# Performance work log

Hardware: AMD Instinct MI355X
Metric: run time of the kernel (lower is better)

## Reference

```python
import jax, jax.numpy as jnp
import numpy as np
import math

# Dims: d_model=192, expand=2 -> d_inner=d_ssm=384, headdim=64 -> nheads=6,
# d_state=128, K=4 scan directions, ngroups=1 (directions fused into state dim).
D_MODEL = 192
D_STATE = 128
D_CONV = 3
EXPAND = 2
HEADDIM = 64
CHUNK = 256
D_INNER = EXPAND * D_MODEL          # 384
D_SSM = D_INNER                     # default d_ssm (d_mlp == 0)
NHEADS = D_SSM // HEADDIM           # 6
K = 4                               # scan directions
HTOT = K * NHEADS                   # 24 heads in the fused scan
NSTATE = K * D_STATE                # 512 fused state dim (ngroups=1)
CONV_BC = 2 * D_STATE + NHEADS      # 262
B, H, W = 2, 64, 64


def _dwconv(x, w, b):
    # x: (B,C,H,W), w: (C,1,k,k) depthwise, SAME padding ((k-1)//2)
    y = jax.lax.conv_general_dilated(
        x, w, (1, 1), [(1, 1), (1, 1)],
        feature_group_count=x.shape[1],
        dimension_numbers=('NCHW', 'OIHW', 'NCHW'))
    return y + b[None, :, None, None]


def _ssd(x, dt_raw, A_logs, Bm, Cm, Ds, dt_bias):
    # Mamba2 chunked selective scan (dt_softplus=True, default dt_limit).
    # x: (b,l,h,p)  dt_raw: (b,l,h)  Bm,Cm: (b,l,n) with ngroups=1
    A = -jnp.exp(A_logs)                              # (h,)
    dt = jax.nn.softplus(dt_raw + dt_bias)            # (b,l,h)
    b, l, h, p = x.shape
    n = Bm.shape[-1]
    nc = l // CHUNK
    xc = x.reshape(b, nc, CHUNK, h, p)
    dtc = dt.reshape(b, nc, CHUNK, h)
    Bc = Bm.reshape(b, nc, CHUNK, n)
    Cc = Cm.reshape(b, nc, CHUNK, n)
    dA = dtc * A                                      # (b,nc,cs,h)
    acum = jnp.cumsum(dA, axis=2)
    # intra-chunk (causal, attention-like)
    a_t = jnp.transpose(acum, (0, 1, 3, 2))           # (b,nc,h,cs)
    diff = a_t[..., :, None] - a_t[..., None, :]      # (b,nc,h,i,j)
    causal = jnp.tril(jnp.ones((CHUNK, CHUNK), bool))
    Lmat = jnp.where(causal, jnp.exp(diff), 0.0)
    CB = jnp.einsum('bcin,bcjn->bcij', Cc, Bc)        # (b,nc,i,j)
    M = CB[:, :, None] * Lmat * jnp.transpose(dtc, (0, 1, 3, 2))[:, :, :, None, :]
    y = jnp.einsum('bchij,bcjhp->bcihp', M, xc)
    # chunk-final states
    decay_end = jnp.exp(acum[:, :, -1:, :] - acum)    # (b,nc,cs,h)
    states = jnp.einsum('bcjh,bcjn,bcjhp->bchpn', decay_end * dtc, Bc, xc)
    chunk_decay = jnp.exp(acum[:, :, -1, :])          # (b,nc,h)

    def step(S, inp):
        st, dec = inp
        return S * dec[:, :, None, None] + st, S

    S0 = jnp.zeros((b, h, p, n), x.dtype)
    _, prev = jax.lax.scan(step, S0, (jnp.moveaxis(states, 1, 0),
                                      jnp.moveaxis(chunk_decay, 1, 0)))
    prev = jnp.moveaxis(prev, 0, 1)                   # (b,nc,h,p,n)
    y = y + jnp.einsum('bcih,bcin,bchpn->bcihp', jnp.exp(acum), Cc, prev)
    y = y + xc * Ds[:, None]                          # D skip connection
    return y.reshape(b, l, h, p)


def _branch(u, u_cross, W_skip, W_xs, W_bcdt, conv_xs_w, conv_xs_b,
            conv_bc_w, conv_bc_b, dt_bias, A_logs, Ds, norm_w, W_out):
    Bb, Hh, Ww, _ = u.shape
    L = Hh * Ww
    z = (u @ W_skip).reshape(Bb, L, D_SSM)            # gate (d_mlp == 0)
    xs = jnp.transpose(u @ W_xs, (0, 3, 1, 2))        # (B,d_ssm,H,W)
    xs = jax.nn.silu(_dwconv(xs, conv_xs_w, conv_xs_b))
    bc = jnp.transpose(u_cross @ W_bcdt, (0, 3, 1, 2))
    bc = jax.nn.silu(_dwconv(bc, conv_bc_w, conv_bc_b))
    xbc = jnp.concatenate([xs, bc], axis=1)           # (B,646,H,W)
    C = xbc.shape[1]
    v = xbc.reshape(Bb, C, L)                         # HW raster
    vt = jnp.transpose(xbc, (0, 1, 3, 2)).reshape(Bb, C, L)  # WH raster
    hw = jnp.stack([v, vt], axis=1)                   # (B,2,C,L)
    xbcdt = jnp.concatenate([hw, jnp.flip(hw, axis=-1)], axis=1)  # (B,4,C,L)
    xp = xbcdt[:, :, :D_SSM]
    Bp = xbcdt[:, :, D_SSM:D_SSM + D_STATE]
    Cp = xbcdt[:, :, D_SSM + D_STATE:D_SSM + 2 * D_STATE]
    dtp = xbcdt[:, :, D_SSM + 2 * D_STATE:]
    x = xp.reshape(Bb, K * D_SSM, L).transpose(0, 2, 1).reshape(Bb, L, HTOT, HEADDIM)
    Bm = Bp.reshape(Bb, NSTATE, L).transpose(0, 2, 1)
    Cm = Cp.reshape(Bb, NSTATE, L).transpose(0, 2, 1)
    dt = dtp.reshape(Bb, HTOT, L).transpose(0, 2, 1)
    y = _ssd(x, dt, A_logs, Bm, Cm, Ds, dt_bias)      # (B,L,24,64)
    y = y.reshape(Bb, L, K, D_SSM)
    out_y = y[:, :, 0]
    inv_y = jnp.flip(y[:, :, 2:4], axis=1)            # (B,L,2,d_ssm)
    wh_y = y[:, :, 1].reshape(Bb, Ww, Hh, D_SSM).transpose(0, 2, 1, 3).reshape(Bb, L, D_SSM)
    invwh_y = inv_y[:, :, 1].reshape(Bb, Ww, Hh, D_SSM).transpose(0, 2, 1, 3).reshape(Bb, L, D_SSM)
    yf = out_y + inv_y[:, :, 0] + wh_y + invwh_y
    # gated RMSNorm (norm_before_gate=False, group_size == d_ssm)
    g = yf * jax.nn.silu(z)
    g = g * jax.lax.rsqrt(jnp.mean(g * g, axis=-1, keepdims=True) + 1e-5) * norm_w
    return (g @ W_out).reshape(Bb, Hh, Ww, D_MODEL)


def setup_inputs():
    key = jax.random.key(0)
    ks = jax.random.split(key, 16)
    f = lambda i, s: jax.random.normal(ks[i], s, jnp.float32)
    sc = 0.02
    dt = jnp.exp(jax.random.uniform(ks[10], (NHEADS,)) *
                 (math.log(0.1) - math.log(0.001)) + math.log(0.001))
    dt = jnp.maximum(dt, 1e-4)
    inv_dt = dt + jnp.log(-jnp.expm1(-dt))
    A = jax.random.uniform(ks[11], (NHEADS,), minval=1.0, maxval=16.0)
    return {
        'u1': f(0, (B, H, W, D_MODEL)),
        'u2': f(1, (B, H, W, D_MODEL)),
        'u2_cat_u1': f(2, (B, H, W, D_MODEL)),
        'u1_cat_u2': f(3, (B, H, W, D_MODEL)),
        'W_skip': f(4, (D_MODEL, D_SSM)) * sc,
        'W_xs': f(5, (D_MODEL, D_SSM)) * sc,
        'W_bcdt': f(6, (D_MODEL, CONV_BC)) * sc,
        'conv_xs_w': f(7, (D_SSM, 1, D_CONV, D_CONV)) * sc,
        'conv_xs_b': jnp.zeros((D_SSM,), jnp.float32),
        'conv_bc_w': f(8, (CONV_BC, 1, D_CONV, D_CONV)) * sc,
        'conv_bc_b': jnp.zeros((CONV_BC,), jnp.float32),
        'dt_bias': jnp.tile(inv_dt, K),
        'A_logs': jnp.tile(jnp.log(A), K),
        'Ds': jnp.ones((HTOT,), jnp.float32),
        'norm_w': jnp.ones((D_SSM,), jnp.float32),
        'W_out': f(9, (D_SSM, D_MODEL)) * sc,
    }


def reference(u1, u2, u2_cat_u1, u1_cat_u2, W_skip, W_xs, W_bcdt,
              conv_xs_w, conv_xs_b, conv_bc_w, conv_bc_b,
              dt_bias, A_logs, Ds, norm_w, W_out):
    args = (W_skip, W_xs, W_bcdt, conv_xs_w, conv_xs_b, conv_bc_w,
            conv_bc_b, dt_bias, A_logs, Ds, norm_w, W_out)
    out1 = _branch(u1, u2_cat_u1, *args)
    out2 = _branch(u2, u1_cat_u2, *args)
    return out1, out2
```

## Files before the change

kernel.cpp:

```cpp
#include <hip/hip_runtime.h>
#include <hip/hip_bf16.h>

#define DEV __device__ __forceinline__

static constexpr int LL   = 4096;
static constexpr int GG   = 4;
static constexpr int CBC  = 262;
static constexpr int BSTR = 264;

typedef float f32x4  __attribute__((ext_vector_type(4)));
typedef short bf16x8 __attribute__((ext_vector_type(8)));
typedef short bf16x4v __attribute__((ext_vector_type(4)));

DEV int map_l(int s, int k) {
    int m = (k & 2) ? (4095 - s) : s;
    if (k & 1) m = ((m & 63) << 6) | (m >> 6);
    return m;
}
DEV float silu_f(float x) { return x / (1.f + __expf(-x)); }
DEV short f2bf(float f) {
    union { __hip_bfloat16 h; short s; } u;
    u.h = __float2bfloat16(f);
    return u.s;
}
DEV float bf2f(short s) {
    return __uint_as_float(((unsigned)(unsigned short)s) << 16);
}
DEV bf16x8 pack8(float4 a, float4 b) {
    bf16x8 r;
    r[0]=f2bf(a.x); r[1]=f2bf(a.y); r[2]=f2bf(a.z); r[3]=f2bf(a.w);
    r[4]=f2bf(b.x); r[5]=f2bf(b.y); r[6]=f2bf(b.z); r[7]=f2bf(b.w);
    return r;
}
DEV bf16x8 load8u(const __hip_bfloat16* p) {
    bf16x4v lo = *(const bf16x4v*)p;
    bf16x4v hi = *(const bf16x4v*)(p + 4);
    bf16x8 r;
    r[0]=lo[0]; r[1]=lo[1]; r[2]=lo[2]; r[3]=lo[3];
    r[4]=hi[0]; r[5]=hi[1]; r[6]=hi[2]; r[7]=hi[3];
    return r;
}
DEV void store16(__hip_bfloat16* p, const float* v) {
    bf16x8 a, b;
    #pragma unroll
    for (int e = 0; e < 8; ++e) { a[e] = f2bf(v[e]); b[e] = f2bf(v[8+e]); }
    *(bf16x8*)p = a;
    *((bf16x8*)p + 1) = b;
}
DEV void storeT(float v, float* p) { *p = v; }
DEV void storeT(float v, __hip_bfloat16* p) { *p = __float2bfloat16(v); }

__global__ void sentinel_k(float* out) { out[0] = 1e30f; }

__global__ void wt_all_k(const float* __restrict__ W_skip, const float* __restrict__ W_xs,
                         const float* __restrict__ W_bcdt, const float* __restrict__ W_out,
                         __hip_bfloat16* __restrict__ Wt)
{
    int idx = blockIdx.x * 256 + threadIdx.x;
    if (idx < 73728) {
        int n = idx / 192, k = idx - n * 192;
        Wt[idx] = __float2bfloat16(W_skip[(size_t)k * 384 + n]);
    } else if (idx < 147456) {
        int r = idx - 73728;
        int n = r / 192, k = r - n * 192;
        Wt[idx] = __float2bfloat16(W_xs[(size_t)k * 384 + n]);
    } else if (idx < 208896) {
        int r = idx - 147456;
        int n = r / 192, k = r - n * 192;
        Wt[idx] = __float2bfloat16(n < 262 ? W_bcdt[(size_t)k * 262 + n] : 0.f);
    } else if (idx < 282624) {
        int r = idx - 208896;
        int n = r / 384, k = r - n * 384;
        Wt[idx] = __float2bfloat16(W_out[(size_t)k * 192 + n]);
    }
}

template<int MODE, typename AT, typename OutT>
__global__ __launch_bounds__(256) void mgemm_k(
    const AT* __restrict__ A0, const AT* __restrict__ A1,
    const __hip_bfloat16* __restrict__ Wt, OutT* __restrict__ C,
    OutT* __restrict__ C2, int N, int Kd)
{
    int i0 = blockIdx.y * 128;
    int j0 = blockIdx.x * 64;
    int t = threadIdx.x;
    int w = t >> 6, lane = t & 63;
    int lr = lane & 15, kq = lane >> 4;
    const AT* arow[2];
    #pragma unroll
    for (int a = 0; a < 2; ++a) {
        int grow = i0 + w * 32 + a * 16 + lr;
        const AT* Ap = (grow < 8192) ? A0 : A1;
        arow[a] = Ap + (size_t)(grow & 8191) * Kd;
    }
    f32x4 acc[2][4] = {};
    for (int k0 = 0; k0 < Kd; k0 += 32) {
        int kb = k0 + kq * 8;
        bf16x8 af[2];
        #pragma unroll
        for (int a = 0; a < 2; ++a) {
            if constexpr (sizeof(AT) == 4)
                af[a] = pack8(*(const float4*)(arow[a] + kb), *(const float4*)(arow[a] + kb + 4));
            else
                af[a] = *(const bf16x8*)(arow[a] + kb);
        }
        #pragma unroll
        for (int b = 0; b < 4; ++b) {
            int n = j0 + b * 16 + lr;
            bf16x8 bfr = *(const bf16x8*)(Wt + (size_t)n * Kd + kb);
            #pragma unroll
            for (int a = 0; a < 2; ++a)
                acc[a][b] = __builtin_amdgcn_mfma_f32_16x16x32_bf16(af[a], bfr, acc[a][b], 0, 0, 0);
        }
    }
    #pragma unroll
    for (int a = 0; a < 2; ++a)
        #pragma unroll
        for (int b = 0; b < 4; ++b)
            #pragma unroll
            for (int r = 0; r < 4; ++r) {
                int row = i0 + w * 32 + a * 16 + kq * 4 + r;
                int col = j0 + b * 16 + lr;
                float v = acc[a][b][r];
                if constexpr (MODE == 0) {
                    if (col < N) storeT(v, &C[(size_t)row * N + col]);
                } else if constexpr (MODE == 1) {
                    if (col < N) storeT(silu_f(v), &C[(size_t)row * N + col]);
                } else {
                    if (col < 384) storeT(silu_f(v), &C[(size_t)row * 384 + col]);
                    else           storeT(v, &C2[(size_t)row * 384 + col - 384]);
                }
            }
}

template<typename InT, typename OutT>
__global__ void dwconv_k(const InT* __restrict__ in, const float* __restrict__ w,
                         const float* __restrict__ bias, OutT* __restrict__ out,
                         int Cin, int Cout)
{
    int idx = blockIdx.x * 256 + threadIdx.x;
    int total = GG * LL * Cin;
    if (idx >= total) return;
    int c = idx % Cin;
    int l = (idx / Cin) % LL;
    int g = idx / (Cin * LL);
    int h = l >> 6, ww = l & 63;
    float acc = bias[c];
    #pragma unroll
    for (int dy = 0; dy < 3; ++dy) {
        int hh = h + dy - 1;
        if ((unsigned)hh >= 64u) continue;
        #pragma unroll
        for (int dx = 0; dx < 3; ++dx) {
            int wx = ww + dx - 1;
            if ((unsigned)wx >= 64u) continue;
            float iv;
            if constexpr (sizeof(InT) == 4) iv = in[((size_t)g * LL + (hh << 6) + wx) * Cin + c];
            else iv = __bfloat162float(in[((size_t)g * LL + (hh << 6) + wx) * Cin + c]);
            acc += iv * w[c * 9 + dy * 3 + dx];
        }
    }
    storeT(silu_f(acc), &out[((size_t)g * LL + l) * Cout + c]);
}

__global__ __launch_bounds__(256) void xtc_k(const __hip_bfloat16* __restrict__ pre_xs,
                                             const float* __restrict__ cxw,
                                             const float* __restrict__ cxb,
                                             __hip_bfloat16* __restrict__ XtG)
{
    __shared__ float raw[18][18][17];
    __shared__ float ls[16][17][17];
    __shared__ float wsm[16][9];
    __shared__ float bsm[16];
    int bid = blockIdx.x;
    int pct = bid % 24;
    int rest = bid / 24;
    int wt = rest & 3, ht2 = (rest >> 2) & 3, g = rest >> 4;
    int h0 = ht2 * 16, w0 = wt * 16, pc0 = pct * 16;
    int t = threadIdx.x;
    if (t < 144) wsm[t / 9][t % 9] = cxw[(pc0 + t / 9) * 9 + t % 9];
    if (t < 16)  bsm[t] = cxb[pc0 + t];
    for (int i = t; i < 18 * 18 * 16; i += 256) {
        int ch = i & 15;
        int hw = i >> 4;
        int ww2 = hw % 18, hh = hw / 18;
        int gh = h0 - 1 + hh, gw = w0 - 1 + ww2;
        float v = 0.f;
        if ((unsigned)gh < 64u && (unsigned)gw < 64u)
            v = __bfloat162float(pre_xs[((size_t)g * LL + gh * 64 + gw) * 384 + pc0 + ch]);
        raw[hh][ww2][ch] = v;
    }
    __syncthreads();
    {
        int h = t >> 4, w2 = t & 15;
        #pragma unroll 4
        for (int ch = 0; ch < 16; ++ch) {
            float acc = bsm[ch];
            #pragma unroll
            for (int dy = 0; dy < 3; ++dy)
                #pragma unroll
                for (int dx = 0; dx < 3; ++dx)
                    acc += raw[h + dy][w2 + dx][ch] * wsm[ch][dy * 3 + dx];
            ls[h][w2][ch] = silu_f(acc);
        }
    }
    __syncthreads();
    int pc = t >> 4, q = t & 15;
    float v[16];
    size_t rowbase;
    #pragma unroll
    for (int e = 0; e < 16; ++e) v[e] = ls[q][e][pc];
    rowbase = ((size_t)(g * 2 + 0) * 384 + pc0 + pc) * 4096;
    store16(XtG + rowbase + (h0 + q) * 64 + w0, v);
    #pragma unroll
    for (int e = 0; e < 16; ++e) v[e] = ls[e][q][pc];
    rowbase = ((size_t)(g * 2 + 1) * 384 + pc0 + pc) * 4096;
    store16(XtG + rowbase + (w0 + q) * 64 + h0, v);
}

__global__ __launch_bounds__(256) void bt_k(const float* __restrict__ bct,
                                            __hip_bfloat16* __restrict__ Bt)
{
    __shared__ float ls[16][17][17];
    int bid = blockIdx.x;
    int nt = bid & 31;
    int rest = bid >> 5;
    int wt = rest & 3, ht2 = (rest >> 2) & 3, g = rest >> 4;
    int h0 = ht2 * 16, w0 = wt * 16;
    int kd = nt >> 3, ch0 = (nt & 7) * 16;
    int t = threadIdx.x;
    int cl = t & 15, hwb = t >> 4;
    #pragma unroll
    for (int r = 0; r < 16; ++r) {
        int hw = hwb + r * 16;
        int h = hw >> 4, w2 = hw & 15;
        ls[h][w2][cl] = bct[((size_t)g * LL + (h0 + h) * 64 + (w0 + w2)) * BSTR + ch0 + cl];
    }
    __syncthreads();
    int pc = t >> 4, q = t & 15;
    int n = nt * 16 + pc;
    __hip_bfloat16* rowp = Bt + ((size_t)g * 512 + n) * 4096;
    float v[16];
    if (kd == 0) {
        #pragma unroll
        for (int e = 0; e < 16; ++e) v[e] = ls[q][e][pc];
        store16(rowp + (h0 + q) * 64 + w0, v);
    } else if (kd == 1) {
        #pragma unroll
        for (int e = 0; e < 16; ++e) v[e] = ls[e][q][pc];
        store16(rowp + (w0 + q) * 64 + h0, v);
    } else if (kd == 2) {
        #pragma unroll
        for (int e = 0; e < 16; ++e) v[e] = ls[q][15 - e][pc];
        store16(rowp + 4095 - (h0 + q) * 64 - w0 - 15, v);
    } else {
        #pragma unroll
        for (int e = 0; e < 16; ++e) v[e] = ls[15 - e][q][pc];
        store16(rowp + 4095 - (w0 + q) * 64 - h0 - 15, v);
    }
}

__global__ __launch_bounds__(256) void cs_k(const float* __restrict__ bct,
                                            __hip_bfloat16* __restrict__ Cs)
{
    __shared__ float ls[16][16][17];
    int bid = blockIdx.x;
    int ct = bid & 15;
    int rest = bid >> 4;
    int wt = rest & 3, ht2 = (rest >> 2) & 3, g = rest >> 4;
    int h0 = ht2 * 16, w0 = wt * 16;
    int kd = ct >> 3, ch0 = (ct & 7) * 16;
    int t = threadIdx.x;
    int cl = t & 15, hwb = t >> 4;
    #pragma unroll
    for (int r = 0; r < 16; ++r) {
        int hw = hwb + r * 16;
        int h = hw >> 4, w2 = hw & 15;
        ls[h][w2][cl] = bct[((size_t)g * LL + (h0 + h) * 64 + (w0 + w2)) * BSTR + 128 + ch0 + cl];
    }
    __syncthreads();
    int h = t >> 4, w2 = t & 15;
    int s = (kd == 0) ? (h0 + h) * 64 + (w0 + w2) : (w0 + w2) * 64 + (h0 + h);
    float v[16];
    #pragma unroll
    for (int e = 0; e < 16; ++e) v[e] = ls[h][w2][e];
    store16(Cs + ((size_t)g * 4096 + s) * 256 + kd * 128 + ch0, v);
}

__global__ __launch_bounds__(256) void dtscan_k(
    const float* __restrict__ bct, const float* __restrict__ dt_bias,
    const float* __restrict__ A_logs, float* __restrict__ dt_arr,
    float* __restrict__ ac_arr, float* __restrict__ cdecay)
{
    int bid = blockIdx.x;
    int ht = bid % 24;
    int gc = bid / 24;
    int c = gc & 15, g = gc >> 4;
    int k = ht / 6, h = ht % 6;
    int t = threadIdx.x;
    int s = c * 256 + t;
    int l = map_l(s, k);
    float raw = bct[((size_t)g * LL + l) * BSTR + 256 + h] + dt_bias[ht];
    float dtv = raw > 20.f ? raw : log1pf(__expf(raw));
    float dA = dtv * (-__expf(A_logs[ht]));
    float v = dA;
    #pragma unroll
    for (int off = 1; off < 64; off <<= 1) {
        float u = __shfl_up(v, off);
        if ((t & 63) >= off) v += u;
    }
    __shared__ float wsum[4];
    if ((t & 63) == 63) wsum[t >> 6] = v;
    __syncthreads();
    float add = 0.f;
    #pragma unroll
    for (int w2 = 0; w2 < 3; ++w2)
        if (w2 < (t >> 6)) add += wsum[w2];
    float cum = v + add;
    size_t base = ((size_t)g * 24 + ht) * LL + s;
    dt_arr[base] = dtv;
    ac_arr[base] = cum;
    if (t == 255) cdecay[(g * 24 + ht) * 16 + c] = __expf(cum);
}

__global__ __launch_bounds__(256) void cb_k(const float* __restrict__ bct,
                                            const __hip_bfloat16* __restrict__ Cs,
                                            __hip_bfloat16* __restrict__ CBm)
{
    int bid = blockIdx.x;
    int jq = bid & 3;
    int gc = bid >> 2;
    int c = gc & 15, g = gc >> 4;
    int t = threadIdx.x;
    int w = t >> 6, lane = t & 63;
    int lr = lane & 15, kq = lane >> 4;
    const float* bg = bct + (size_t)g * LL * BSTR;
    const __hip_bfloat16* cg = Cs + (size_t)g * 4096 * 256;
    f32x4 acc[4][4] = {};
    for (int ks = 0; ks < 16; ++ks) {
        int n0 = ks * 32 + kq * 8;
        int kd = n0 >> 7, nn = n0 & 127;
        bf16x8 bfr[4];
        #pragma unroll
        for (int jt = 0; jt < 4; ++jt) {
            int j = jq * 64 + jt * 16 + lr;
            int l = map_l(c * 256 + j, kd);
            const float* p = bg + (size_t)l * BSTR + nn;
            bfr[jt] = pack8(*(const float4*)p, *(const float4*)(p + 4));
        }
        #pragma unroll
        for (int iq = 0; iq < 4; ++iq) {
            int i = (w * 4 + iq) * 16 + lr;
            int s = c * 256 + i;
            int row = (kd < 2) ? s : 4095 - s;
            int col = ((kd & 1) << 7) + nn;
            bf16x8 af = *(const bf16x8*)(cg + (size_t)row * 256 + col);
            #pragma unroll
            for (int jt = 0; jt < 4; ++jt)
                acc[iq][jt] = __builtin_amdgcn_mfma_f32_16x16x32_bf16(af, bfr[jt], acc[iq][jt], 0, 0, 0);
        }
    }
    __hip_bfloat16* ob = CBm + (size_t)gc * 65536;
    #pragma unroll
    for (int iq = 0; iq < 4; ++iq)
        #pragma unroll
        for (int jt = 0; jt < 4; ++jt)
            #pragma unroll
            for (int r = 0; r < 4; ++r) {
                int i = (w * 4 + iq) * 16 + kq * 4 + r;
                int j = jq * 64 + jt * 16 + lr;
                ob[(size_t)i * 256 + j] = __float2bfloat16(acc[iq][jt][r]);
            }
}

__global__ __launch_bounds__(256) void states_k(
    const __hip_bfloat16* __restrict__ XtG, const __hip_bfloat16* __restrict__ Bt,
    const float* __restrict__ dt_arr, const float* __restrict__ ac_arr,
    __hip_bfloat16* __restrict__ states)
{
    __shared__ float wsh[256];
    __shared__ short xw[64][264];
    int task = (blockIdx.x & 7) * 192 + (blockIdx.x >> 3);
    int ht = task % 24;
    int gc = task / 24;
    int c = gc & 15, g = gc >> 4;
    int kd = ht / 6;
    bool rev = kd >= 2;
    int c0 = (ht % 6) * 64;
    int t = threadIdx.x;
    int w = t >> 6, lane = t & 63;
    int lr = lane & 15, kq = lane >> 4;
    const float* dtp = dt_arr + ((size_t)g * 24 + ht) * LL + c * 256;
    const float* acp = ac_arr + ((size_t)g * 24 + ht) * LL + c * 256;
    float ac_last = acp[255];
    wsh[t] = __expf(ac_last - acp[t]) * dtp[t];
    __syncthreads();
    const __hip_bfloat16* xg = XtG + ((size_t)(g * 2 + (kd & 1)) * 384 + c0) * 4096;
    #pragma unroll
    for (int r8 = 0; r8 < 8; ++r8) {
        int id = t + 256 * r8;
        int p = id >> 5;
        int jc = (id & 31) * 8;
        bf16x8 xv;
        if (!rev) {
            xv = *(const bf16x8*)(xg + (size_t)p * 4096 + c * 256 + jc);
        } else {
            bf16x8 tmp = load8u(xg + (size_t)p * 4096 + 4088 - c * 256 - jc);
            #pragma unroll
            for (int e = 0; e < 8; ++e) xv[e] = tmp[7 - e];
        }
        bf16x8 o;
        #pragma unroll
        for (int e = 0; e < 8; ++e) o[e] = f2bf(bf2f(xv[e]) * wsh[jc + e]);
        *(bf16x8*)&xw[p][jc] = o;
    }
    __syncthreads();
    const __hip_bfloat16* btg = Bt + (size_t)g * 512 * 4096;
    f32x4 acc[4][8] = {};
    for (int ks = 0; ks < 8; ++ks) {
        int j0 = ks * 32 + kq * 8;
        bf16x8 af[4];
        #pragma unroll
        for (int pt = 0; pt < 4; ++pt)
            af[pt] = *(const bf16x8*)&xw[pt * 16 + lr][j0];
        #pragma unroll
        for (int nt = 0; nt < 8; ++nt) {
            int n = (w * 8 + nt) * 16 + lr;
            bf16x8 bv = *(const bf16x8*)(btg + (size_t)n * 4096 + c * 256 + j0);
            #pragma unroll
            for (int pt = 0; pt < 4; ++pt)
                acc[pt][nt] = __builtin_amdgcn_mfma_f32_16x16x32_bf16(af[pt], bv, acc[pt][nt], 0, 0, 0);
        }
    }
    __hip_bfloat16* ob = states + ((size_t)gc * 24 + ht) * 32768;
    #pragma unroll
    for (int pt = 0; pt < 4; ++pt)
        #pragma unroll
        for (int nt = 0; nt < 8; ++nt)
            #pragma unroll
            for (int r = 0; r < 4; ++r) {
                int p = pt * 16 + kq * 4 + r;
                int n = (w * 8 + nt) * 16 + lr;
                ob[(size_t)p * 512 + n] = __float2bfloat16(acc[pt][nt][r]);
            }
}

__global__ void scan_k(__hip_bfloat16* __restrict__ states, const float* __restrict__ cdecay)
{
    int idx = blockIdx.x * 256 + threadIdx.x;
    int g = idx / 786432;
    int r = idx - g * 786432;
    int ht = r >> 15;
    int pn = r & 32767;
    const float* cd = cdecay + (g * 24 + ht) * 16;
    __hip_bfloat16* base = states + ((size_t)g * 384 + ht) * 32768 + pn;
    float S = 0.f;
    #pragma unroll
    for (int c2 = 0; c2 < 16; ++c2) {
        __hip_bfloat16* p = base + (size_t)c2 * 786432;
        float tmp = __bfloat162float(*p);
        *p = __float2bfloat16(S);
        S = S * cd[c2] + tmp;
    }
}

__global__ __launch_bounds__(256) void yk(
    const __hip_bfloat16* __restrict__ XtG, const __hip_bfloat16* __restrict__ Cs,
    const __hip_bfloat16* __restrict__ CBm, const __hip_bfloat16* __restrict__ prev,
    const float* __restrict__ dt_arr, const float* __restrict__ ac_arr,
    const float* __restrict__ Ds, __hip_bfloat16* __restrict__ y4)
{
    __shared__ float acs[256], dts[256], ejdt[256];
    __shared__ short xl[64][264];
    int task = (blockIdx.x & 7) * 192 + (blockIdx.x >> 3);
    int ht = task % 24;
    int gc = task / 24;
    int c = gc & 15, g = gc >> 4;
    int kd = ht / 6;
    bool rev = kd >= 2;
    int c0 = (ht % 6) * 64;
    int t = threadIdx.x;
    int w = t >> 6, lane = t & 63;
    int lr = lane & 15, kq = lane >> 4;
    acs[t] = ac_arr[((size_t)g * 24 + ht) * LL + c * 256 + t];
    dts[t] = dt_arr[((size_t)g * 24 + ht) * LL + c * 256 + t];
    const __hip_bfloat16* xg = XtG + ((size_t)(g * 2 + (kd & 1)) * 384 + c0) * 4096;
    #pragma unroll
    for (int r8 = 0; r8 < 8; ++r8) {
        int id = t + 256 * r8;
        int p = id >> 5;
        int jc = (id & 31) * 8;
        bf16x8 xv;
        if (!rev) {
            xv = *(const bf16x8*)(xg + (size_t)p * 4096 + c * 256 + jc);
        } else {
            bf16x8 tmp = load8u(xg + (size_t)p * 4096 + 4088 - c * 256 - jc);
            #pragma unroll
            for (int e = 0; e < 8; ++e) xv[e] = tmp[7 - e];
        }
        *(bf16x8*)&xl[p][jc] = xv;
    }
    __syncthreads();
    ejdt[t] = __expf(acs[t & ~31] - acs[t]) * dts[t];
    __syncthreads();
    const __hip_bfloat16* cbb = CBm + (size_t)gc * 65536;
    const __hip_bfloat16* cg = Cs + (size_t)g * 4096 * 256;
    f32x4 acc[4][4] = {};
    const __hip_bfloat16* pv = prev + ((size_t)gc * 24 + ht) * 32768;
    auto ld2 = [&](int ns, bf16x8* afq, bf16x8* pb) {
        int n0 = ns * 32 + kq * 8;
        int kd2 = n0 >> 7, nn = n0 & 127;
        int col = ((kd2 & 1) << 7) + nn;
        #pragma unroll
        for (int q = 0; q < 4; ++q) {
            int i = (w + 4 * q) * 16 + lr;
            int s = c * 256 + i;
            int row = (kd2 < 2) ? s : 4095 - s;
            afq[q] = *(const bf16x8*)(cg + (size_t)row * 256 + col);
        }
        #pragma unroll
        for (int pt = 0; pt < 4; ++pt)
            pb[pt] = *(const bf16x8*)(pv + (size_t)(pt * 16 + lr) * 512 + n0);
    };
    auto fma2 = [&](bf16x8* afq, bf16x8* pb) {
        #pragma unroll
        for (int q = 0; q < 4; ++q)
            #pragma unroll
            for (int pt = 0; pt < 4; ++pt)
                acc[q][pt] = __builtin_amdgcn_mfma_f32_16x16x32_bf16(afq[q], pb[pt], acc[q][pt], 0, 0, 0);
    };
    {
        bf16x8 afA[4], pbA[4], afB[4], pbB[4];
        ld2(0, afA, pbA);
        #pragma unroll
        for (int ns = 0; ns < 16; ns += 2) {
            if (ns + 1 < 16) ld2(ns + 1, afB, pbB);
            fma2(afA, pbA);
            if (ns + 2 < 16) ld2(ns + 2, afA, pbA);
            fma2(afB, pbB);
        }
    }
    #pragma unroll
    for (int q = 0; q < 4; ++q)
        #pragma unroll
        for (int r = 0; r < 4; ++r) {
            float er = __expf(acs[(w + 4 * q) * 16 + kq * 4 + r]);
            #pragma unroll
            for (int pt = 0; pt < 4; ++pt) acc[q][pt][r] *= er;
        }
    float aci_q[4];
    #pragma unroll
    for (int q = 0; q < 4; ++q) aci_q[q] = acs[(w + 4 * q) * 16 + lr];
    for (int ks = 0; ks < 8; ++ks) {
        int j0 = ks * 32 + kq * 8;
        bf16x8 xb[4];
        #pragma unroll
        for (int pt = 0; pt < 4; ++pt)
            xb[pt] = *(const bf16x8*)&xl[pt * 16 + lr][j0];
        float acb = acs[ks * 32];
        float ej[8];
        #pragma unroll
        for (int e = 0; e < 8; ++e) ej[e] = ejdt[j0 + e];
        #pragma unroll
        for (int q = 0; q < 4; ++q) {
            int rt = w + 4 * q;
            if (rt < 2 * ks) continue;
            int i = rt * 16 + lr;
            float r2 = __expf(aci_q[q] - acb);
            bf16x8 cb8 = *(const bf16x8*)(cbb + (size_t)i * 256 + j0);
            bf16x8 af;
            if (rt >= 2 * ks + 2) {
                #pragma unroll
                for (int e = 0; e < 8; ++e)
                    af[e] = f2bf(r2 * ej[e] * bf2f(cb8[e]));
            } else {
                #pragma unroll
                for (int e = 0; e < 8; ++e) {
                    float coef = r2 * ej[e] * bf2f(cb8[e]);
                    af[e] = (j0 + e <= i) ? f2bf(coef) : (short)0;
                }
            }
            #pragma unroll
            for (int pt = 0; pt < 4; ++pt)
                acc[q][pt] = __builtin_amdgcn_mfma_f32_16x16x32_bf16(af, xb[pt], acc[q][pt], 0, 0, 0);
        }
    }
    float Dsv = Ds[ht];
    __hip_bfloat16* yb = y4 + (((size_t)(g * 4 + kd) * 4096 + c * 256) * 384) + c0;
    #pragma unroll
    for (int q = 0; q < 4; ++q) {
        int rt = w + 4 * q;
        #pragma unroll
        for (int pt = 0; pt < 4; ++pt) {
            int p = pt * 16 + lr;
            int ibase = rt * 16 + kq * 4;
            bf16x4v x4 = *(const bf16x4v*)&xl[p][ibase];
            #pragma unroll
            for (int r = 0; r < 4; ++r) {
                int i = ibase + r;
                float xv = bf2f(x4[r]);
                yb[(size_t)i * 384 + p] = __float2bfloat16(acc[q][pt][r] + Dsv * xv);
            }
        }
    }
}

__global__ __launch_bounds__(128) void gate_k(
    const __hip_bfloat16* __restrict__ y4, const __hip_bfloat16* __restrict__ z_silu,
    const float* __restrict__ norm_w, __hip_bfloat16* __restrict__ gn)
{
    int g = blockIdx.x >> 12;
    int l = blockIdx.x & 4095;
    int t = threadIdx.x;
    int Tl = ((l & 63) << 6) | (l >> 6);
    const __hip_bfloat16* p0 = y4 + ((size_t)(g * 4 + 0) * 4096 + l) * 384;
    const __hip_bfloat16* p1 = y4 + ((size_t)(g * 4 + 1) * 4096 + Tl) * 384;
    const __hip_bfloat16* p2 = y4 + ((size_t)(g * 4 + 2) * 4096 + 4095 - l) * 384;
    const __hip_bfloat16* p3 = y4 + ((size_t)(g * 4 + 3) * 4096 + 4095 - Tl) * 384;
    const __hip_bfloat16* zp = z_silu + ((size_t)g * LL + l) * 384;
    float gc[3]; float ssq = 0.f;
    #pragma unroll
    for (int q = 0; q < 3; ++q) {
        int cdim = t + 128 * q;
        float yf = __bfloat162float(p0[cdim]) + __bfloat162float(p1[cdim]) +
                   __bfloat162float(p2[cdim]) + __bfloat162float(p3[cdim]);
        float v = yf * __bfloat162float(zp[cdim]);
        gc[q] = v;
        ssq += v * v;
    }
    float v = ssq;
    #pragma unroll
    for (int off = 32; off > 0; off >>= 1) v += __shfl_down(v, off);
    __shared__ float tot[2];
    if ((t & 63) == 0) tot[t >> 6] = v;
    __syncthreads();
    float rs = rsqrtf((tot[0] + tot[1]) * (1.f / 384.f) + 1e-5f);
    __hip_bfloat16* gp = gn + ((size_t)g * LL + l) * 384;
    #pragma unroll
    for (int q = 0; q < 3; ++q) {
        int cdim = t + 128 * q;
        gp[cdim] = __float2bfloat16(gc[q] * rs * norm_w[cdim]);
    }
}

extern "C" void kernel_launch(void* const* d_in, const int* in_sizes, int n_in,
                              void* d_out, int out_size, void* d_ws, size_t ws_size,
                              hipStream_t stream)
{
    const float* u1      = (const float*)d_in[0];
    const float* u2      = (const float*)d_in[1];
    const float* u21     = (const float*)d_in[2];
    const float* u12     = (const float*)d_in[3];
    const float* W_skip  = (const float*)d_in[4];
    const float* W_xs    = (const float*)d_in[5];
    const float* W_bcdt  = (const float*)d_in[6];
    const float* cxw     = (const float*)d_in[7];
    const float* cxb     = (const float*)d_in[8];
    const float* cbw     = (const float*)d_in[9];
    const float* cbb     = (const float*)d_in[10];
    const float* dt_bias = (const float*)d_in[11];
    const float* A_logs  = (const float*)d_in[12];
    const float* Ds      = (const float*)d_in[13];
    const float* norm_w  = (const float*)d_in[14];
    const float* W_out   = (const float*)d_in[15];
    float* out = (float*)d_out;

    char* w = (char*)d_ws;
    size_t o_y4  = 0;
    size_t o_st  = o_y4 + 50331648;
    size_t o_z   = o_st + 100663296;
    size_t o_xtg = o_z  + 12582912;
    size_t o_bt  = o_xtg + 25165824;
    size_t o_cs  = o_bt + 16777216;
    size_t o_cbm = o_cs + 8388608;
    size_t o_dt  = o_cbm + 8388608;
    size_t o_ac  = o_dt + 1572864;
    size_t o_cd  = o_ac + 1572864;
    size_t o_wt  = o_cd + 8192;
    size_t total = o_wt + 589824;
    if (total > ws_size) {
        sentinel_k<<<1, 1, 0, stream>>>(out);
        return;
    }
    __hip_bfloat16* y4     = (__hip_bfloat16*)(w + o_y4);
    __hip_bfloat16* states = (__hip_bfloat16*)(w + o_st);
    __hip_bfloat16* z_silu = (__hip_bfloat16*)(w + o_z);
    __hip_bfloat16* XtG    = (__hip_bfloat16*)(w + o_xtg);
    __hip_bfloat16* Bt     = (__hip_bfloat16*)(w + o_bt);
    __hip_bfloat16* Cs     = (__hip_bfloat16*)(w + o_cs);
    __hip_bfloat16* CBm    = (__hip_bfloat16*)(w + o_cbm);
    float*          dt_arr = (float*)(w + o_dt);
    float*          ac_arr = (float*)(w + o_ac);
    float*          cdecay = (float*)(w + o_cd);
    __hip_bfloat16* Wt     = (__hip_bfloat16*)(w + o_wt);
    __hip_bfloat16* Wt_skip = Wt;
    __hip_bfloat16* Wt_bcdt = Wt + 147456;
    __hip_bfloat16* Wt_out  = Wt + 208896;
    float*          bct    = (float*)(w + o_y4);
    __hip_bfloat16* pre_bc = (__hip_bfloat16*)(w + o_st);
    __hip_bfloat16* pre_xs = (__hip_bfloat16*)(w + o_st + 8650752);
    __hip_bfloat16* gn     = (__hip_bfloat16*)(w + o_st);

    dim3 blk(256);
    wt_all_k<<<dim3(1104), blk, 0, stream>>>(W_skip, W_xs, W_bcdt, W_out, Wt);
    mgemm_k<2, float, __hip_bfloat16><<<dim3(12, 128), blk, 0, stream>>>(
        u1, u2, Wt_skip, z_silu, pre_xs, 768, 192);
    mgemm_k<0, float, __hip_bfloat16><<<dim3(5, 128), blk, 0, stream>>>(
        u21, u12, Wt_bcdt, pre_bc, nullptr, CBC, 192);
    dwconv_k<__hip_bfloat16, float><<<dim3((GG * LL * CBC) / 256), blk, 0, stream>>>(
        pre_bc, cbw, cbb, bct, CBC, BSTR);
    xtc_k<<<dim3(1536), blk, 0, stream>>>(pre_xs, cxw, cxb, XtG);
    bt_k<<<dim3(2048), blk, 0, stream>>>(bct, Bt);
    cs_k<<<dim3(1024), blk, 0, stream>>>(bct, Cs);
    dtscan_k<<<dim3(1536), blk, 0, stream>>>(bct, dt_bias, A_logs, dt_arr, ac_arr, cdecay);
    cb_k<<<dim3(256), blk, 0, stream>>>(bct, Cs, CBm);
    states_k<<<dim3(1536), blk, 0, stream>>>(XtG, Bt, dt_arr, ac_arr, states);
    scan_k<<<dim3(12288), blk, 0, stream>>>(states, cdecay);
    yk<<<dim3(1536), blk, 0, stream>>>(XtG, Cs, CBm, states, dt_arr, ac_arr, Ds, y4);
    gate_k<<<dim3(16384), dim3(128), 0, stream>>>(y4, z_silu, norm_w, gn);
    mgemm_k<0, __hip_bfloat16, float><<<dim3(3, 128), blk, 0, stream>>>(
        gn, gn + (size_t)8192 * 384, Wt_out, out, nullptr, 192, 384);
}
```

Measured before the change: 459.5 us.

## Fuse B/C transpose and dt-scan prep kernels; add bf16 B layout for CB GEMM

Merges bt_k, cs_k and dtscan_k into a single prep_k launch selected by block index, and has it also write a bf16 copy of B in the same row layout as C. cb_k then reads contiguous bf16 vectors instead of gathering scattered fp32 rows through map_l. In states_k and yk the X loads are issued earlier into registers so they overlap with the dt/ac loads, and yk computes the chunk-base cumsum with a shuffle, dropping one barrier. In exchange it needs an extra 8 MB workspace buffer and more register pressure from holding X in registers.

```diff
diff --git a/kernel.cpp b/kernel.cpp
--- a/kernel.cpp
+++ b/kernel.cpp
@@ -218,113 +218,110 @@
     store16(XtG + rowbase + (w0 + q) * 64 + h0, v);
 }
 
-__global__ __launch_bounds__(256) void bt_k(const float* __restrict__ bct,
-                                            __hip_bfloat16* __restrict__ Bt)
+__global__ __launch_bounds__(256) void prep_k(
+    const float* __restrict__ bct, const float* __restrict__ dt_bias,
+    const float* __restrict__ A_logs, __hip_bfloat16* __restrict__ Bt,
+    __hip_bfloat16* __restrict__ Cs, __hip_bfloat16* __restrict__ Bs,
+    float* __restrict__ dt_arr, float* __restrict__ ac_arr,
+    float* __restrict__ cdecay)
 {
     __shared__ float ls[16][17][17];
+    __shared__ float wsum[4];
     int bid = blockIdx.x;
-    int nt = bid & 31;
-    int rest = bid >> 5;
-    int wt = rest & 3, ht2 = (rest >> 2) & 3, g = rest >> 4;
-    int h0 = ht2 * 16, w0 = wt * 16;
-    int kd = nt >> 3, ch0 = (nt & 7) * 16;
     int t = threadIdx.x;
-    int cl = t & 15, hwb = t >> 4;
-    #pragma unroll
-    for (int r = 0; r < 16; ++r) {
-        int hw = hwb + r * 16;
-        int h = hw >> 4, w2 = hw & 15;
-        ls[h][w2][cl] = bct[((size_t)g * LL + (h0 + h) * 64 + (w0 + w2)) * BSTR + ch0 + cl];
-    }
-    __syncthreads();
-    int pc = t >> 4, q = t & 15;
-    int n = nt * 16 + pc;
-    __hip_bfloat16* rowp = Bt + ((size_t)g * 512 + n) * 4096;
-    float v[16];
-    if (kd == 0) {
-        #pragma unroll
-        for (int e = 0; e < 16; ++e) v[e] = ls[q][e][pc];
-        store16(rowp + (h0 + q) * 64 + w0, v);
-    } else if (kd == 1) {
-        #pragma unroll
-        for (int e = 0; e < 16; ++e) v[e] = ls[e][q][pc];
-        store16(rowp + (w0 + q) * 64 + h0, v);
-    } else if (kd == 2) {
-        #pragma unroll
-        for (int e = 0; e < 16; ++e) v[e] = ls[q][15 - e][pc];
-        store16(rowp + 4095 - (h0 + q) * 64 - w0 - 15, v);
+    if (bid < 2048) {
+        int nt = bid & 31;
+        int rest = bid >> 5;
+        int wt = rest & 3, ht2 = (rest >> 2) & 3, g = rest >> 4;
+        int h0 = ht2 * 16, w0 = wt * 16;
+        int kd = nt >> 3, ch0 = (nt & 7) * 16;
+        int cl = t & 15, hwb = t >> 4;
+        #pragma unroll
+        for (int r = 0; r < 16; ++r) {
+            int hw = hwb + r * 16;
+            int h = hw >> 4, w2 = hw & 15;
+            ls[h][w2][cl] = bct[((size_t)g * LL + (h0 + h) * 64 + (w0 + w2)) * BSTR + ch0 + cl];
+        }
+        __syncthreads();
+        int pc = t >> 4, q = t & 15;
+        int n = nt * 16 + pc;
+        __hip_bfloat16* rowp = Bt + ((size_t)g * 512 + n) * 4096;
+        float v[16];
+        if (kd == 0) {
+            #pragma unroll
+            for (int e = 0; e < 16; ++e) v[e] = ls[q][e][pc];
+            store16(rowp + (h0 + q) * 64 + w0, v);
+        } else if (kd == 1) {
+            #pragma unroll
+            for (int e = 0; e < 16; ++e) v[e] = ls[e][q][pc];
+            store16(rowp + (w0 + q) * 64 + h0, v);
+        } else if (kd == 2) {
+            #pragma unroll
+            for (int e = 0; e < 16; ++e) v[e] = ls[q][15 - e][pc];
+            store16(rowp + 4095 - (h0 + q) * 64 - w0 - 15, v);
+        } else {
+            #pragma unroll
+            for (int e = 0; e < 16; ++e) v[e] = ls[15 - e][q][pc];
+            store16(rowp + 4095 - (w0 + q) * 64 - h0 - 15, v);
+        }
+    } else if (bid < 4096) {
+        int b2 = bid - 2048;
+        int ct = b2 & 31;
+        int rest = b2 >> 5;
+        int wt = rest & 3, ht2 = (rest >> 2) & 3, g = rest >> 4;
+        int h0 = ht2 * 16, w0 = wt * 16;
+        bool isB = ct >= 16;
+        int ctl = ct & 15;
+        int kd = ctl >> 3, ch0 = (ctl & 7) * 16;
+        int off = (isB ? 0 : 128) + ch0;
+        __hip_bfloat16* dst = isB ? Bs : Cs;
+        int cl = t & 15, hwb = t >> 4;
+        #pragma unroll
+        for (int r = 0; r < 16; ++r) {
+            int hw = hwb + r * 16;
+            int h = hw >> 4, w2 = hw & 15;
+            ls[h][w2][cl] = bct[((size_t)g * LL + (h0 + h) * 64 + (w0 + w2)) * BSTR + off + cl];
+        }
+        __syncthreads();
+        int h = t >> 4, w2 = t & 15;
+        int s = (kd == 0) ? (h0 + h) * 64 + (w0 + w2) : (w0 + w2) * 64 + (h0 + h);
+        float v[16];
+        #pragma unroll
+        for (int e = 0; e < 16; ++e) v[e] = ls[h][w2][e];
+        store16(dst + ((size_t)g * 4096 + s) * 256 + kd * 128 + ch0, v);
     } else {
-        #pragma unroll
-        for (int e = 0; e < 16; ++e) v[e] = ls[15 - e][q][pc];
-        store16(rowp + 4095 - (w0 + q) * 64 - h0 - 15, v);
-    }
-}
-
-__global__ __launch_bounds__(256) void cs_k(const float* __restrict__ bct,
-                                            __hip_bfloat16* __restrict__ Cs)
-{
-    __shared__ float ls[16][16][17];
-    int bid = blockIdx.x;
-    int ct = bid & 15;
-    int rest = bid >> 4;
-    int wt = rest & 3, ht2 = (rest >> 2) & 3, g = rest >> 4;
-    int h0 = ht2 * 16, w0 = wt * 16;
-    int kd = ct >> 3, ch0 = (ct & 7) * 16;
-    int t = threadIdx.x;
-    int cl = t & 15, hwb = t >> 4;
-    #pragma unroll
-    for (int r = 0; r < 16; ++r) {
-        int hw = hwb + r * 16;
-        int h = hw >> 4, w2 = hw & 15;
-        ls[h][w2][cl] = bct[((size_t)g * LL + (h0 + h) * 64 + (w0 + w2)) * BSTR + 128 + ch0 + cl];
-    }
-    __syncthreads();
-    int h = t >> 4, w2 = t & 15;
-    int s = (kd == 0) ? (h0 + h) * 64 + (w0 + w2) : (w0 + w2) * 64 + (h0 + h);
-    float v[16];
-    #pragma unroll
-    for (int e = 0; e < 16; ++e) v[e] = ls[h][w2][e];
-    store16(Cs + ((size_t)g * 4096 + s) * 256 + kd * 128 + ch0, v);
-}
-
-__global__ __launch_bounds__(256) void dtscan_k(
-    const float* __restrict__ bct, const float* __restrict__ dt_bias,
-    const float* __restrict__ A_logs, float* __restrict__ dt_arr,
-    float* __restrict__ ac_arr, float* __restrict__ cdecay)
-{
-    int bid = blockIdx.x;
-    int ht = bid % 24;
-    int gc = bid / 24;
-    int c = gc & 15, g = gc >> 4;
-    int k = ht / 6, h = ht % 6;
-    int t = threadIdx.x;
-    int s = c * 256 + t;
-    int l = map_l(s, k);
-    float raw = bct[((size_t)g * LL + l) * BSTR + 256 + h] + dt_bias[ht];
-    float dtv = raw > 20.f ? raw : log1pf(__expf(raw));
-    float dA = dtv * (-__expf(A_logs[ht]));
-    float v = dA;
-    #pragma unroll
-    for (int off = 1; off < 64; off <<= 1) {
-        float u = __shfl_up(v, off);
-        if ((t & 63) >= off) v += u;
-    }
-    __shared__ float wsum[4];
-    if ((t & 63) == 63) wsum[t >> 6] = v;
-    __syncthreads();
-    float add = 0.f;
-    #pragma unroll
-    for (int w2 = 0; w2 < 3; ++w2)
-        if (w2 < (t >> 6)) add += wsum[w2];
-    float cum = v + add;
-    size_t base = ((size_t)g * 24 + ht) * LL + s;
-    dt_arr[base] = dtv;
-    ac_arr[base] = cum;
-    if (t == 255) cdecay[(g * 24 + ht) * 16 + c] = __expf(cum);
-}
-
-__global__ __launch_bounds__(256) void cb_k(const float* __restrict__ bct,
-                                            const __hip_bfloat16* __restrict__ Cs,
+        int b3 = bid - 4096;
+        int ht = b3 % 24;
+        int gc = b3 / 24;
+        int c = gc & 15, g = gc >> 4;
+        int k = ht / 6, h = ht % 6;
+        int s = c * 256 + t;
+        int l = map_l(s, k);
+        float raw = bct[((size_t)g * LL + l) * BSTR + 256 + h] + dt_bias[ht];
+        float dtv = raw > 20.f ? raw : log1pf(__expf(raw));
+        float dA = dtv * (-__expf(A_logs[ht]));
+        float v = dA;
+        #pragma unroll
+        for (int off = 1; off < 64; off <<= 1) {
+            float u = __shfl_up(v, off);
+            if ((t & 63) >= off) v += u;
+        }
+        if ((t & 63) == 63) wsum[t >> 6] = v;
+        __syncthreads();
+        float add = 0.f;
+        #pragma unroll
+        for (int w2 = 0; w2 < 3; ++w2)
+            if (w2 < (t >> 6)) add += wsum[w2];
+        float cum = v + add;
+        size_t base = ((size_t)g * 24 + ht) * LL + s;
+        dt_arr[base] = dtv;
+        ac_arr[base] = cum;
+        if (t == 255) cdecay[(g * 24 + ht) * 16 + c] = __expf(cum);
+    }
+}
+
+__global__ __launch_bounds__(256) void cb_k(const __hip_bfloat16* __restrict__ Cs,
+                                            const __hip_bfloat16* __restrict__ Bs,
                                             __hip_bfloat16* __restrict__ CBm)
 {
     int bid = blockIdx.x;
@@ -334,26 +331,26 @@
     int t = threadIdx.x;
     int w = t >> 6, lane = t & 63;
     int lr = lane & 15, kq = lane >> 4;
-    const float* bg = bct + (size_t)g * LL * BSTR;
     const __hip_bfloat16* cg = Cs + (size_t)g * 4096 * 256;
+    const __hip_bfloat16* bsg = Bs + (size_t)g * 4096 * 256;
     f32x4 acc[4][4] = {};
     for (int ks = 0; ks < 16; ++ks) {
         int n0 = ks * 32 + kq * 8;
         int kd = n0 >> 7, nn = n0 & 127;
+        int col = ((kd & 1) << 7) + nn;
         bf16x8 bfr[4];
         #pragma unroll
         for (int jt = 0; jt < 4; ++jt) {
             int j = jq * 64 + jt * 16 + lr;
-            int l = map_l(c * 256 + j, kd);
-            const float* p = bg + (size_t)l * BSTR + nn;
-            bfr[jt] = pack8(*(const float4*)p, *(const float4*)(p + 4));
+            int s = c * 256 + j;
+            int row = (kd < 2) ? s : 4095 - s;
+            bfr[jt] = *(const bf16x8*)(bsg + (size_t)row * 256 + col);
         }
         #pragma unroll
         for (int iq = 0; iq < 4; ++iq) {
             int i = (w * 4 + iq) * 16 + lr;
             int s = c * 256 + i;
             int row = (kd < 2) ? s : 4095 - s;
-            int col = ((kd & 1) << 7) + nn;
             bf16x8 af = *(const bf16x8*)(cg + (size_t)row * 256 + col);
             #pragma unroll
             for (int jt = 0; jt < 4; ++jt)
@@ -390,28 +387,32 @@
     int t = threadIdx.x;
     int w = t >> 6, lane = t & 63;
     int lr = lane & 15, kq = lane >> 4;
+    const __hip_bfloat16* xg = XtG + ((size_t)(g * 2 + (kd & 1)) * 384 + c0) * 4096;
+    bf16x8 xr[8];
+    #pragma unroll
+    for (int r8 = 0; r8 < 8; ++r8) {
+        int id = t + 256 * r8;
+        int p = id >> 5;
+        int jc = (id & 31) * 8;
+        xr[r8] = rev ? load8u(xg + (size_t)p * 4096 + 4088 - c * 256 - jc)
+                     : *(const bf16x8*)(xg + (size_t)p * 4096 + c * 256 + jc);
+    }
     const float* dtp = dt_arr + ((size_t)g * 24 + ht) * LL + c * 256;
     const float* acp = ac_arr + ((size_t)g * 24 + ht) * LL + c * 256;
     float ac_last = acp[255];
     wsh[t] = __expf(ac_last - acp[t]) * dtp[t];
     __syncthreads();
-    const __hip_bfloat16* xg = XtG + ((size_t)(g * 2 + (kd & 1)) * 384 + c0) * 4096;
     #pragma unroll
     for (int r8 = 0; r8 < 8; ++r8) {
         int id = t + 256 * r8;
         int p = id >> 5;
         int jc = (id & 31) * 8;
-        bf16x8 xv;
-        if (!rev) {
-            xv = *(const bf16x8*)(xg + (size_t)p * 4096 + c * 256 + jc);
-        } else {
-            bf16x8 tmp = load8u(xg + (size_t)p * 4096 + 4088 - c * 256 - jc);
-            #pragma unroll
-            for (int e = 0; e < 8; ++e) xv[e] = tmp[7 - e];
-        }
         bf16x8 o;
         #pragma unroll
-        for (int e = 0; e < 8; ++e) o[e] = f2bf(bf2f(xv[e]) * wsh[jc + e]);
+        for (int e = 0; e < 8; ++e) {
+            short xe = rev ? xr[r8][7 - e] : xr[r8][e];
+            o[e] = f2bf(bf2f(xe) * wsh[jc + e]);
+        }
         *(bf16x8*)&xw[p][jc] = o;
     }
     __syncthreads();
@@ -482,27 +483,23 @@
     int t = threadIdx.x;
     int w = t >> 6, lane = t & 63;
     int lr = lane & 15, kq = lane >> 4;
-    acs[t] = ac_arr[((size_t)g * 24 + ht) * LL + c * 256 + t];
-    dts[t] = dt_arr[((size_t)g * 24 + ht) * LL + c * 256 + t];
     const __hip_bfloat16* xg = XtG + ((size_t)(g * 2 + (kd & 1)) * 384 + c0) * 4096;
+    bf16x8 xr[8];
     #pragma unroll
     for (int r8 = 0; r8 < 8; ++r8) {
         int id = t + 256 * r8;
         int p = id >> 5;
         int jc = (id & 31) * 8;
-        bf16x8 xv;
-        if (!rev) {
-            xv = *(const bf16x8*)(xg + (size_t)p * 4096 + c * 256 + jc);
-        } else {
-            bf16x8 tmp = load8u(xg + (size_t)p * 4096 + 4088 - c * 256 - jc);
-            #pragma unroll
-            for (int e = 0; e < 8; ++e) xv[e] = tmp[7 - e];
-        }
-        *(bf16x8*)&xl[p][jc] = xv;
-    }
-    __syncthreads();
-    ejdt[t] = __expf(acs[t & ~31] - acs[t]) * dts[t];
-    __syncthreads();
+        xr[r8] = rev ? load8u(xg + (size_t)p * 4096 + 4088 - c * 256 - jc)
+                     : *(const bf16x8*)(xg + (size_t)p * 4096 + c * 256 + jc);
+    }
+    size_t abase = ((size_t)g * 24 + ht) * LL + c * 256;
+    float ac_own = ac_arr[abase + t];
+    float dt_own = dt_arr[abase + t];
+    acs[t] = ac_own;
+    dts[t] = dt_own;
+    float acb0 = __shfl(ac_own, (t & 63) & ~31);
+    ejdt[t] = __expf(acb0 - ac_own) * dt_own;
     const __hip_bfloat16* cbb = CBm + (size_t)gc * 65536;
     const __hip_bfloat16* cg = Cs + (size_t)g * 4096 * 256;
     f32x4 acc[4][4] = {};
@@ -540,6 +537,19 @@
             fma2(afB, pbB);
         }
     }
+    #pragma unroll
+    for (int r8 = 0; r8 < 8; ++r8) {
+        int id = t + 256 * r8;
+        int p = id >> 5;
+        int jc = (id & 31) * 8;
+        bf16x8 o;
+        if (rev) {
+            #pragma unroll
+            for (int e = 0; e < 8; ++e) o[e] = xr[r8][7 - e];
+        } else o = xr[r8];
+        *(bf16x8*)&xl[p][jc] = o;
+    }
+    __syncthreads();
     #pragma unroll
     for (int q = 0; q < 4; ++q)
         #pragma unroll
@@ -677,7 +687,8 @@
     size_t o_ac  = o_dt + 1572864;
     size_t o_cd  = o_ac + 1572864;
     size_t o_wt  = o_cd + 8192;
-    size_t total = o_wt + 589824;
+    size_t o_bs  = o_wt + 589824;
+    size_t total = o_bs + 8388608;
     if (total > ws_size) {
         sentinel_k<<<1, 1, 0, stream>>>(out);
         return;
@@ -693,6 +704,7 @@
     float*          ac_arr = (float*)(w + o_ac);
     float*          cdecay = (float*)(w + o_cd);
     __hip_bfloat16* Wt     = (__hip_bfloat16*)(w + o_wt);
+    __hip_bfloat16* Bs     = (__hip_bfloat16*)(w + o_bs);
     __hip_bfloat16* Wt_skip = Wt;
     __hip_bfloat16* Wt_bcdt = Wt + 147456;
     __hip_bfloat16* Wt_out  = Wt + 208896;
@@ -710,10 +722,9 @@
     dwconv_k<__hip_bfloat16, float><<<dim3((GG * LL * CBC) / 256), blk, 0, stream>>>(
         pre_bc, cbw, cbb, bct, CBC, BSTR);
     xtc_k<<<dim3(1536), blk, 0, stream>>>(pre_xs, cxw, cxb, XtG);
-    bt_k<<<dim3(2048), blk, 0, stream>>>(bct, Bt);
-    cs_k<<<dim3(1024), blk, 0, stream>>>(bct, Cs);
-    dtscan_k<<<dim3(1536), blk, 0, stream>>>(bct, dt_bias, A_logs, dt_arr, ac_arr, cdecay);
-    cb_k<<<dim3(256), blk, 0, stream>>>(bct, Cs, CBm);
+    prep_k<<<dim3(5632), blk, 0, stream>>>(bct, dt_bias, A_logs, Bt, Cs, Bs,
+                                           dt_arr, ac_arr, cdecay);
+    cb_k<<<dim3(256), blk, 0, stream>>>(Cs, Bs, CBm);
     states_k<<<dim3(1536), blk, 0, stream>>>(XtG, Bt, dt_arr, ac_arr, states);
     scan_k<<<dim3(12288), blk, 0, stream>>>(states, cdecay);
     yk<<<dim3(1536), blk, 0, stream>>>(XtG, Cs, CBm, states, dt_arr, ac_arr, Ds, y4);
```

After: 491.0 us. 6.8% more time.
